# Kernel tuning notes

Measured on AMD Instinct MI355X. Metric: run time of the kernel, lower is better.

The kernel has to match this reference:

```python
import jax, jax.numpy as jnp
import numpy as np

# pywt 'db2' filter bank (decomposition and reconstruction), float32
DEC_LO = jnp.array([-0.12940952255092145, 0.22414386804185735, 0.836516303737469, 0.48296291314469025], dtype=jnp.float32)
DEC_HI = jnp.array([-0.48296291314469025, 0.836516303737469, -0.22414386804185735, -0.12940952255092145], dtype=jnp.float32)
REC_LO = jnp.array([0.48296291314469025, 0.836516303737469, 0.22414386804185735, -0.12940952255092145], dtype=jnp.float32)
REC_HI = jnp.array([-0.12940952255092145, -0.22414386804185735, 0.836516303737469, -0.48296291314469025], dtype=jnp.float32)
_FLEN = 4
_DN = ('NCW', 'OIW', 'NCW')


def _convolve(x, f, stride, padding, lhs_dilation=1):
    # np.convolve-style convolution (kernel flipped) along last axis; x: (B, n)
    k = f[::-1][None, None, :]
    y = jax.lax.conv_general_dilated(x[:, None, :], k, (stride,), padding,
                                     lhs_dilation=(lhs_dilation,),
                                     dimension_numbers=_DN)
    return y[:, 0, :]


def _dwt_db2(x):
    # pywt.dwt(x, 'db2', mode='symmetric') along last axis; n even.
    # symmetric extension by flen-1=3 on each side, valid convolution, take odd indices.
    ext = jnp.concatenate([x[:, 2::-1], x, x[:, -1:-4:-1]], axis=1)[:, 1:]
    cA = _convolve(ext, DEC_LO, 2, 'VALID')  # (B, n/2+1)
    cD = _convolve(ext, DEC_HI, 2, 'VALID')
    return cA, cD


def _idwt_db2(cA, cD):
    # pywt.idwt(cA, cD, 'db2'): upsample-by-2 convolution with rec filters,
    # trimmed to length 2L - flen + 2. Equivalent to lhs_dilation=2, pad (1,1).
    lo = _convolve(cA, REC_LO, 1, [(1, 1)], lhs_dilation=2)
    hi = _convolve(cD, REC_HI, 1, [(1, 1)], lhs_dilation=2)
    return lo + hi  # (B, n)


def setup_inputs() -> dict:
    key = jax.random.key(0)
    k1, k2 = jax.random.split(key)
    B, D = 65536, 512
    x = jax.random.normal(k1, (B, D), dtype=jnp.float32)
    weight = jax.random.normal(k2, (2, D // 2 + 1), dtype=jnp.float32)
    return {"x": x, "weight": weight}


def reference(x, weight):
    shape = x.shape
    x2 = x.reshape(-1, shape[-1])
    cA, cD = _dwt_db2(x2)
    z = _idwt_db2(cA, weight[0] * cD)
    return jax.nn.leaky_relu(z.reshape(shape), negative_slope=0.01)
```

## Files before the change

kernel.cpp:

```cpp
#include <hip/hip_runtime.h>
#include <stdint.h>


#define N 512

typedef float f4v __attribute__((ext_vector_type(4)));

__device__ __forceinline__ void row_compute(
    const f4v va, const f4v vb,
    const float xl0, const float xl1, const float xr0, const float xr1,
    const f4v wv, const float w4,
    f4v& oa, f4v& ob)
{
    constexpr float DL0 = -0.12940952255092145f, DL1 = 0.22414386804185735f,
                    DL2 =  0.836516303737469f,   DL3 = 0.48296291314469025f;
    constexpr float DH0 = -0.48296291314469025f, DH1 = 0.836516303737469f,
                    DH2 = -0.22414386804185735f, DH3 = -0.12940952255092145f;
    constexpr float RL0 =  0.48296291314469025f, RL1 = 0.836516303737469f,
                    RL2 =  0.22414386804185735f, RL3 = -0.12940952255092145f;
    constexpr float RH0 = -0.12940952255092145f, RH1 = -0.22414386804185735f,
                    RH2 =  0.836516303737469f,   RH3 = -0.48296291314469025f;

    float A0 = DL3*xl0  + DL2*xl1  + DL1*va.x + DL0*va.y;
    float D0 = DH3*xl0  + DH2*xl1  + DH1*va.x + DH0*va.y;
    float A1 = DL3*va.x + DL2*va.y + DL1*va.z + DL0*va.w;
    float D1 = DH3*va.x + DH2*va.y + DH1*va.z + DH0*va.w;
    float A2 = DL3*va.z + DL2*va.w + DL1*vb.x + DL0*vb.y;
    float D2 = DH3*va.z + DH2*va.w + DH1*vb.x + DH0*vb.y;
    float A3 = DL3*vb.x + DL2*vb.y + DL1*vb.z + DL0*vb.w;
    float D3 = DH3*vb.x + DH2*vb.y + DH1*vb.z + DH0*vb.w;
    float A4 = DL3*vb.z + DL2*vb.w + DL1*xr0  + DL0*xr1;
    float D4 = DH3*vb.z + DH2*vb.w + DH1*xr0  + DH0*xr1;

    D0 *= wv.x; D1 *= wv.y; D2 *= wv.z; D3 *= wv.w; D4 *= w4;

    float z0 = RL2*A0 + RL0*A1 + RH2*D0 + RH0*D1;
    float z1 = RL3*A0 + RL1*A1 + RH3*D0 + RH1*D1;
    float z2 = RL2*A1 + RL0*A2 + RH2*D1 + RH0*D2;
    float z3 = RL3*A1 + RL1*A2 + RH3*D1 + RH1*D2;
    float z4 = RL2*A2 + RL0*A3 + RH2*D2 + RH0*D3;
    float z5 = RL3*A2 + RL1*A3 + RH3*D2 + RH1*D3;
    float z6 = RL2*A3 + RL0*A4 + RH2*D3 + RH0*D4;
    float z7 = RL3*A3 + RL1*A4 + RH3*D3 + RH1*D4;

    oa.x = fmaxf(z0, 0.f) + 0.01f * fminf(z0, 0.f);
    oa.y = fmaxf(z1, 0.f) + 0.01f * fminf(z1, 0.f);
    oa.z = fmaxf(z2, 0.f) + 0.01f * fminf(z2, 0.f);
    oa.w = fmaxf(z3, 0.f) + 0.01f * fminf(z3, 0.f);
    ob.x = fmaxf(z4, 0.f) + 0.01f * fminf(z4, 0.f);
    ob.y = fmaxf(z5, 0.f) + 0.01f * fminf(z5, 0.f);
    ob.z = fmaxf(z6, 0.f) + 0.01f * fminf(z6, 0.f);
    ob.w = fmaxf(z7, 0.f) + 0.01f * fminf(z7, 0.f);
}

__device__ __forceinline__ void halo(
    const f4v va, const f4v vb, const int lane,
    float& xl0, float& xl1, float& xr0, float& xr1)
{
    xl0 = __shfl_up(vb.z, 1);
    xl1 = __shfl_up(vb.w, 1);
    xr0 = __shfl_down(va.x, 1);
    xr1 = __shfl_down(va.y, 1);
    if (lane == 0)  { xl0 = va.y; xl1 = va.x; }
    if (lane == 63) { xr0 = vb.w; xr1 = vb.z; }
}

#define DO_ROW(VA, VB, BASE)                                            \
    do {                                                                \
        float xl0, xl1, xr0, xr1;                                       \
        f4v oa, ob;                                                     \
        halo(VA, VB, lane, xl0, xl1, xr0, xr1);                         \
        row_compute(VA, VB, xl0, xl1, xr0, xr1, wv, w4, oa, ob);        \
        __builtin_nontemporal_store(oa, (f4v*)(out + (BASE)));          \
        __builtin_nontemporal_store(ob, (f4v*)(out + (BASE) + 4));      \
    } while (0)

__global__ __launch_bounds__(256) void wavelet_kernel(
    const float* __restrict__ x,
    const float* __restrict__ w,
    float* __restrict__ out,
    int nrows)
{
    const int lane = threadIdx.x & 63;
    const int wid  = threadIdx.x >> 6;

    const f4v  wv = *(const f4v*)(w + 4 * lane);
    const float w4 = w[4 * lane + 4];

    const int octet = (int)blockIdx.x * 4 + wid;
    const int r0 = octet * 8;
    if (r0 >= nrows) return;

    const size_t base0 = (size_t)r0 * N + ((size_t)lane << 3);

    if (r0 + 8 <= nrows) {
        f4v va0 = *(const f4v*)(x + base0);
        f4v vb0 = *(const f4v*)(x + base0 + 4);
        f4v va1 = *(const f4v*)(x + base0 + 1 * N);
        f4v vb1 = *(const f4v*)(x + base0 + 1 * N + 4);
        f4v va2 = *(const f4v*)(x + base0 + 2 * N);
        f4v vb2 = *(const f4v*)(x + base0 + 2 * N + 4);
        f4v va3 = *(const f4v*)(x + base0 + 3 * N);
        f4v vb3 = *(const f4v*)(x + base0 + 3 * N + 4);
        f4v va4 = *(const f4v*)(x + base0 + 4 * N);
        f4v vb4 = *(const f4v*)(x + base0 + 4 * N + 4);
        f4v va5 = *(const f4v*)(x + base0 + 5 * N);
        f4v vb5 = *(const f4v*)(x + base0 + 5 * N + 4);
        f4v va6 = *(const f4v*)(x + base0 + 6 * N);
        f4v vb6 = *(const f4v*)(x + base0 + 6 * N + 4);
        f4v va7 = *(const f4v*)(x + base0 + 7 * N);
        f4v vb7 = *(const f4v*)(x + base0 + 7 * N + 4);

        DO_ROW(va0, vb0, base0);
        DO_ROW(va1, vb1, base0 + 1 * N);
        DO_ROW(va2, vb2, base0 + 2 * N);
        DO_ROW(va3, vb3, base0 + 3 * N);
        DO_ROW(va4, vb4, base0 + 4 * N);
        DO_ROW(va5, vb5, base0 + 5 * N);
        DO_ROW(va6, vb6, base0 + 6 * N);
        DO_ROW(va7, vb7, base0 + 7 * N);
    } else {
        for (int r = r0; r < nrows; ++r) {
            const size_t b = (size_t)r * N + ((size_t)lane << 3);
            f4v va = *(const f4v*)(x + b);
            f4v vb = *(const f4v*)(x + b + 4);
            DO_ROW(va, vb, b);
        }
    }
}

extern "C" void kernel_launch(void* const* d_in, const int* in_sizes, int n_in,
                              void* d_out, int out_size, void* d_ws, size_t ws_size,
                              hipStream_t stream) {
    const float* x = (const float*)d_in[0];
    const float* w = (const float*)d_in[1];
    float* out = (float*)d_out;

    const int nrows = in_sizes[0] / N;
    const int octets = (nrows + 7) / 8;
    int blocks = (octets + 3) / 4;
    if (blocks < 1) blocks = 1;
    wavelet_kernel<<<blocks, 256, 0, stream>>>(x, w, out, nrows);
}
```

Baseline: 242.4 us.

## Software-pipeline row loads across four-row groups with 16 rows per wave

Each wave now handles 16 rows in four groups of four. The loads for the next group are issued behind a scheduling barrier before the current group is computed, so global loads overlap with compute. Nontemporal stores become ordinary stores and the grid is halved. The kernel is memory bound, so the gain depends on whether the extra per-wave latency hiding outweighs having fewer waves in flight, and ordinary stores may pollute the cache.

```diff
diff --git a/kernel.cpp b/kernel.cpp
--- a/kernel.cpp
+++ b/kernel.cpp
@@ -71,8 +71,36 @@
         f4v oa, ob;                                                     \
         halo(VA, VB, lane, xl0, xl1, xr0, xr1);                         \
         row_compute(VA, VB, xl0, xl1, xr0, xr1, wv, w4, oa, ob);        \
-        __builtin_nontemporal_store(oa, (f4v*)(out + (BASE)));          \
-        __builtin_nontemporal_store(ob, (f4v*)(out + (BASE) + 4));      \
+        *(f4v*)(out + (BASE))     = oa;                                 \
+        *(f4v*)(out + (BASE) + 4) = ob;                                 \
+    } while (0)
+
+#define PREFETCH(NB)                                                    \
+    do {                                                                \
+        na0 = *(const f4v*)(x + (NB));                                  \
+        nb0 = *(const f4v*)(x + (NB) + 4);                              \
+        na1 = *(const f4v*)(x + (NB) + 1 * N);                          \
+        nb1 = *(const f4v*)(x + (NB) + 1 * N + 4);                      \
+        na2 = *(const f4v*)(x + (NB) + 2 * N);                          \
+        nb2 = *(const f4v*)(x + (NB) + 2 * N + 4);                      \
+        na3 = *(const f4v*)(x + (NB) + 3 * N);                          \
+        nb3 = *(const f4v*)(x + (NB) + 3 * N + 4);                      \
+        __builtin_amdgcn_sched_barrier(0);                              \
+    } while (0)
+
+#define COMPUTE_CUR()                                                   \
+    do {                                                                \
+        DO_ROW(ca0, cb0, base);                                         \
+        DO_ROW(ca1, cb1, base + 1 * N);                                 \
+        DO_ROW(ca2, cb2, base + 2 * N);                                 \
+        DO_ROW(ca3, cb3, base + 3 * N);                                 \
+    } while (0)
+
+#define ROTATE(NB)                                                      \
+    do {                                                                \
+        ca0 = na0; cb0 = nb0; ca1 = na1; cb1 = nb1;                     \
+        ca2 = na2; cb2 = nb2; ca3 = na3; cb3 = nb3;                     \
+        base = (NB);                                                    \
     } while (0)
 
 __global__ __launch_bounds__(256) void wavelet_kernel(
@@ -87,44 +115,49 @@
     const f4v  wv = *(const f4v*)(w + 4 * lane);
     const float w4 = w[4 * lane + 4];
 
-    const int octet = (int)blockIdx.x * 4 + wid;
-    const int r0 = octet * 8;
+    const int wave_id = (int)blockIdx.x * 4 + wid;
+    const int r0 = wave_id * 16;
     if (r0 >= nrows) return;
 
-    const size_t base0 = (size_t)r0 * N + ((size_t)lane << 3);
+    size_t base = (size_t)r0 * N + ((size_t)lane << 3);
 
-    if (r0 + 8 <= nrows) {
-        f4v va0 = *(const f4v*)(x + base0);
-        f4v vb0 = *(const f4v*)(x + base0 + 4);
-        f4v va1 = *(const f4v*)(x + base0 + 1 * N);
-        f4v vb1 = *(const f4v*)(x + base0 + 1 * N + 4);
-        f4v va2 = *(const f4v*)(x + base0 + 2 * N);
-        f4v vb2 = *(const f4v*)(x + base0 + 2 * N + 4);
-        f4v va3 = *(const f4v*)(x + base0 + 3 * N);
-        f4v vb3 = *(const f4v*)(x + base0 + 3 * N + 4);
-        f4v va4 = *(const f4v*)(x + base0 + 4 * N);
-        f4v vb4 = *(const f4v*)(x + base0 + 4 * N + 4);
-        f4v va5 = *(const f4v*)(x + base0 + 5 * N);
-        f4v vb5 = *(const f4v*)(x + base0 + 5 * N + 4);
-        f4v va6 = *(const f4v*)(x + base0 + 6 * N);
-        f4v vb6 = *(const f4v*)(x + base0 + 6 * N + 4);
-        f4v va7 = *(const f4v*)(x + base0 + 7 * N);
-        f4v vb7 = *(const f4v*)(x + base0 + 7 * N + 4);
+    if (r0 + 16 <= nrows) {
+        f4v ca0 = *(const f4v*)(x + base);
+        f4v cb0 = *(const f4v*)(x + base + 4);
+        f4v ca1 = *(const f4v*)(x + base + 1 * N);
+        f4v cb1 = *(const f4v*)(x + base + 1 * N + 4);
+        f4v ca2 = *(const f4v*)(x + base + 2 * N);
+        f4v cb2 = *(const f4v*)(x + base + 2 * N + 4);
+        f4v ca3 = *(const f4v*)(x + base + 3 * N);
+        f4v cb3 = *(const f4v*)(x + base + 3 * N + 4);
+        __builtin_amdgcn_sched_barrier(0);
 
-        DO_ROW(va0, vb0, base0);
-        DO_ROW(va1, vb1, base0 + 1 * N);
-        DO_ROW(va2, vb2, base0 + 2 * N);
-        DO_ROW(va3, vb3, base0 + 3 * N);
-        DO_ROW(va4, vb4, base0 + 4 * N);
-        DO_ROW(va5, vb5, base0 + 5 * N);
-        DO_ROW(va6, vb6, base0 + 6 * N);
-        DO_ROW(va7, vb7, base0 + 7 * N);
+        f4v na0, nb0, na1, nb1, na2, nb2, na3, nb3;
+
+        PREFETCH(base + 4 * N);
+        COMPUTE_CUR();
+        ROTATE(base + 4 * N);
+
+        PREFETCH(base + 4 * N);
+        COMPUTE_CUR();
+        ROTATE(base + 4 * N);
+
+        PREFETCH(base + 4 * N);
+        COMPUTE_CUR();
+        ROTATE(base + 4 * N);
+
+        COMPUTE_CUR();
     } else {
         for (int r = r0; r < nrows; ++r) {
             const size_t b = (size_t)r * N + ((size_t)lane << 3);
             f4v va = *(const f4v*)(x + b);
             f4v vb = *(const f4v*)(x + b + 4);
-            DO_ROW(va, vb, b);
+            float xl0, xl1, xr0, xr1;
+            f4v oa, ob;
+            halo(va, vb, lane, xl0, xl1, xr0, xr1);
+            row_compute(va, vb, xl0, xl1, xr0, xr1, wv, w4, oa, ob);
+            *(f4v*)(out + b)     = oa;
+            *(f4v*)(out + b + 4) = ob;
         }
     }
 }
@@ -137,8 +170,8 @@
     float* out = (float*)d_out;
 
     const int nrows = in_sizes[0] / N;
-    const int octets = (nrows + 7) / 8;
-    int blocks = (octets + 3) / 4;
+    const int waves = (nrows + 15) / 16;
+    int blocks = (waves + 3) / 4;
     if (blocks < 1) blocks = 1;
     wavelet_kernel<<<blocks, 256, 0, stream>>>(x, w, out, nrows);
 }
```

After: 233.7 us. -3.6%, faster.
